# Kernel tuning notes

Hardware: AMD Instinct MI355X
Metric: run time of the kernel (lower is better)

The kernel has to match this reference:

```python
import jax, jax.numpy as jnp
import numpy as np

N = 8192          # total nodes (bipartite: first half left, second half right)
E = 65536         # raw edges
D = 256           # emb_dim
H = 8             # heads
HD = D // H       # head_dim = 32
EAD = 2           # edge_attr_dim


def _init(k, shape, fan_in):
    return (jax.random.normal(k, shape, jnp.float32) / np.sqrt(fan_in)).astype(jnp.float32)


def setup_inputs() -> dict:
    key = jax.random.key(0)
    ks = jax.random.split(key, 16)
    x = jax.random.normal(ks[0], (N, D), jnp.float32)
    src = jax.random.randint(ks[1], (E,), 0, N // 2, jnp.int32)
    dst = jax.random.randint(ks[2], (E,), N // 2, N, jnp.int32)
    edge_index = jnp.stack([src, dst])                       # [2, E]
    edge_attr = jax.random.uniform(ks[3], (E, EAD), jnp.float32)
    query_mask = jax.random.randint(ks[4], (E,), 0, 2, jnp.int32).astype(bool)
    return {
        "x": x,
        "edge_index": edge_index,
        "edge_attr": edge_attr,
        "query_mask": query_mask,
        "start_right": N // 2,
        "W_kqv": _init(ks[5], (D, 3 * D), D), "b_kqv": jnp.zeros((3 * D,), jnp.float32),
        "W_edge": _init(ks[6], (EAD, D), EAD), "b_edge": jnp.zeros((D,), jnp.float32),
        "W_att1": _init(ks[7], (3 * HD, HD), 3 * HD), "b_att1": jnp.zeros((HD,), jnp.float32),
        "W_att2": _init(ks[8], (HD, 1), HD), "b_att2": jnp.zeros((1,), jnp.float32),
        "W_out": _init(ks[9], (D, D), D), "b_out": jnp.zeros((D,), jnp.float32),
        "bn_gamma": jnp.ones((D,), jnp.float32), "bn_beta": jnp.zeros((D,), jnp.float32),
    }


def _build_graph(edge_index, query_mask, n):
    """Replicates MetaGNN.forward edge preprocessing (static, int-only)."""
    ei = np.asarray(edge_index)
    qm = np.asarray(query_mask).astype(bool)
    sup = np.where(~qm)[0]                                   # support edges
    # cat([edge_index[:, support], edge_index.flip(0)], dim=1)
    src = np.concatenate([ei[0, sup], ei[1]])
    dst = np.concatenate([ei[1, sup], ei[0]])
    attr_idx = np.concatenate([sup, np.arange(ei.shape[1])])
    # remove_self_loops
    keep = src != dst
    src, dst, attr_idx = src[keep], dst[keep], attr_idx[keep]
    # add_self_loops with fill_value [0, 0]
    loops = np.arange(n)
    src = np.concatenate([src, loops])
    dst = np.concatenate([dst, loops])
    return jnp.asarray(src), jnp.asarray(dst), jnp.asarray(attr_idx)


def _layer(x, src, dst, ea, W_kqv, b_kqv, W_edge, b_edge, W_att1, b_att1,
           W_att2, b_att2, W_out, b_out, bn_gamma, bn_beta):
    n = x.shape[0]
    kqv = x @ W_kqv + b_kqv                                  # [N, 3D]
    q = kqv[dst, :D].reshape(-1, H, HD)                      # x_i (target)
    k = kqv[src, D:2 * D].reshape(-1, H, HD) / np.sqrt(HD)   # x_j (source)
    v = kqv[src, 2 * D:].reshape(-1, H, HD)
    ef = jax.nn.relu((ea @ W_edge + b_edge).reshape(-1, H, HD))
    feat = jnp.concatenate([k, q, ef], axis=-1)              # [E, H, 3*HD]
    hdn = jax.nn.relu(jnp.einsum('ehf,fd->ehd', feat, W_att1) + b_att1)
    logits = (jnp.einsum('ehd,do->eho', hdn, W_att2) + b_att2)[..., 0]  # [E, H]
    # scatter-softmax over destination node segments
    m = jax.ops.segment_max(logits, dst, num_segments=n)
    a = jnp.exp(logits - m[dst])
    s = jax.ops.segment_sum(a, dst, num_segments=n)
    alpha = a / (s[dst] + 1e-16)                             # [E, H]
    msg = (alpha[..., None] * v).reshape(-1, D) @ W_out + b_out
    out = jax.ops.segment_sum(msg, dst, num_segments=n) + x  # aggr='add' + residual
    # BatchNorm1d (training-mode batch statistics, eps=1e-5)
    mu = out.mean(axis=0)
    var = out.var(axis=0)
    return (out - mu) / jnp.sqrt(var + 1e-5) * bn_gamma + bn_beta


def reference(x, edge_index, edge_attr, query_mask, start_right,
              W_kqv, b_kqv, W_edge, b_edge, W_att1, b_att1, W_att2, b_att2,
              W_out, b_out, bn_gamma, bn_beta):
    n = x.shape[0]
    src, dst, attr_idx = _build_graph(edge_index, query_mask, n)
    ea = jnp.concatenate(
        [edge_attr[attr_idx], jnp.zeros((n, edge_attr.shape[1]), edge_attr.dtype)], axis=0)
    return _layer(x, src, dst, ea, W_kqv, b_kqv, W_edge, b_edge,
                  W_att1, b_att1, W_att2, b_att2, W_out, b_out, bn_gamma, bn_beta)
```

## Files before the change

kernel.cpp:

```cpp
#include <hip/hip_runtime.h>

#define N_NODES 8192
#define E_RAW   65536
#define NSLOT   (2*E_RAW + N_NODES)
#define DEGCAP  48
#define L_ITER  4
#define MAIN_BLKS (E_RAW / (8 * L_ITER))
#define TAIL_BLKS (N_NODES / (8 * L_ITER))

typedef __attribute__((ext_vector_type(8)))  short bf16x8;
typedef __attribute__((ext_vector_type(4)))  short bf16x4;
typedef __attribute__((ext_vector_type(4)))  float f32x4;
typedef __attribute__((ext_vector_type(16))) float f32x16;
typedef unsigned short u16;

__device__ __forceinline__ u16 f2b(float f) {
  unsigned u = __float_as_uint(f);
  u = (u + 0x7FFFu + ((u >> 16) & 1u)) >> 16;
  return (u16)u;
}
__device__ __forceinline__ float b2f(u16 b) {
  return __uint_as_float(((unsigned)b) << 16);
}

__device__ __forceinline__ bf16x4 kq_rd(const char* wbase, int p, int h, int off) {
  int byte = (p*512 + h*64 + off*2) ^ ((p & 7) << 4);
  return *(const bf16x4*)(wbase + byte);
}

__global__ __launch_bounds__(256) void setup_k(
    const float* __restrict__ x, u16* __restrict__ xb,
    const float* __restrict__ W_kqv, const float* __restrict__ b_kqv,
    const float* __restrict__ W_att1, const float* __restrict__ b_att1,
    const float* __restrict__ W_edge, const float* __restrict__ b_edge,
    const float* __restrict__ W_out,
    u16* __restrict__ BcatT, float* __restrict__ biascat,
    u16* __restrict__ wa1t, u16* __restrict__ WoutT, float* __restrict__ beW,
    int4* __restrict__ zbase)
{
  __shared__ float tile[64][65];
  const float inv_sqrt_hd = 0.17677669529663687f;
  int bx = blockIdx.x, t = threadIdx.x;

  if (bx < 2048) {
    int i = bx * 256 + t;
    float4 v = ((const float4*)x)[i];
    ushort4 o;
    o.x = f2b(v.x); o.y = f2b(v.y); o.z = f2b(v.z); o.w = f2b(v.w);
    ((ushort4*)xb)[i] = o;
    return;
  }
  if (bx < 2836) {
    int c = bx - 2048;
    int i = t;
    if (c < 768) {
      float v;
      if (c < 256) {
        int h = c >> 5, d2 = c & 31;
        float s = 0.f;
        #pragma unroll
        for (int j = 0; j < 32; ++j)
          s += W_kqv[i*768 + 256 + h*32 + j] * W_att1[j*32 + d2];
        v = s * inv_sqrt_hd;
      } else if (c < 512) {
        int c2 = c - 256; int h = c2 >> 5, d2 = c2 & 31;
        float s = 0.f;
        #pragma unroll
        for (int j = 0; j < 32; ++j)
          s += W_kqv[i*768 + h*32 + j] * W_att1[(32+j)*32 + d2];
        v = s;
      } else {
        v = W_kqv[i*768 + c];
      }
      BcatT[(size_t)c * 256 + i] = f2b(v);
      if (i == 0) {
        float bv;
        if (c < 256) {
          int h = c >> 5, d2 = c & 31;
          float s = 0.f;
          for (int j = 0; j < 32; ++j)
            s += b_kqv[256 + h*32 + j] * W_att1[j*32 + d2];
          bv = s * inv_sqrt_hd;
        } else if (c < 512) {
          int c2 = c - 256; int h = c2 >> 5, d2 = c2 & 31;
          float s = 0.f;
          for (int j = 0; j < 32; ++j)
            s += b_kqv[h*32 + j] * W_att1[(32+j)*32 + d2];
          bv = s + b_att1[c2 & 31];
        } else {
          bv = b_kqv[c];
        }
        biascat[c] = bv;
      }
    } else if (c < 772) {
      int idx = (c - 768) * 256 + i;
      int d2 = idx >> 5, j = idx & 31;
      wa1t[idx] = f2b(W_att1[(64 + j) * 32 + d2]);
    } else {
      int b = c - 772;
      int r0 = (b >> 2) * 64, c0 = (b & 3) * 64;
      for (int idx = i; idx < 4096; idx += 256) {
        int r = idx >> 6, cc = idx & 63;
        tile[r][cc] = W_out[(size_t)(r0 + r) * 256 + c0 + cc];
      }
      __syncthreads();
      for (int idx = i; idx < 4096; idx += 256) {
        int cc = idx >> 6, r = idx & 63;
        WoutT[(size_t)(c0 + cc) * 256 + r0 + r] = f2b(tile[r][cc]);
      }
    }
    return;
  }
  if (bx == 2836) {
    int h = t >> 5, d2 = t & 31;
    float s = 0.f;
    #pragma unroll
    for (int f = 0; f < 32; ++f)
      s += fmaxf(b_edge[h*32 + f], 0.f) * W_att1[(64 + f)*32 + d2];
    beW[h*32 + d2] = s;
    return;
  }
  int i = (bx - 2837) * 256 + t;
  if (i < 2176) zbase[i] = make_int4(0, 0, 0, 0);
}

__global__ __launch_bounds__(256) void gemm_scatter_k(
    const u16* __restrict__ xb, const u16* __restrict__ BcatT,
    const float* __restrict__ biascat, u16* __restrict__ nodeF,
    const int* __restrict__ ei, const int* __restrict__ qm,
    int* __restrict__ cnt, int* __restrict__ csr)
{
  int bx = blockIdx.x, t = threadIdx.x;
  if (bx < 768) {
    int lane = t & 63, wid = t >> 6;
    int cb = bx % 12, rb = bx / 12;
    int r0 = rb * 128 + wid * 32;
    int c0 = cb * 64;
    int lr = lane & 15, lk = (lane >> 4) * 8;
    f32x4 acc0[4] = {}, acc1[4] = {};
    for (int k0 = 0; k0 < 256; k0 += 32) {
      bf16x8 a0 = *(const bf16x8*)&xb[(size_t)(r0 + lr) * 256 + k0 + lk];
      bf16x8 a1 = *(const bf16x8*)&xb[(size_t)(r0 + 16 + lr) * 256 + k0 + lk];
      bf16x8 b0 = *(const bf16x8*)&BcatT[(size_t)(c0 + lr) * 256 + k0 + lk];
      bf16x8 b1 = *(const bf16x8*)&BcatT[(size_t)(c0 + 16 + lr) * 256 + k0 + lk];
      bf16x8 b2 = *(const bf16x8*)&BcatT[(size_t)(c0 + 32 + lr) * 256 + k0 + lk];
      bf16x8 b3 = *(const bf16x8*)&BcatT[(size_t)(c0 + 48 + lr) * 256 + k0 + lk];
      acc0[0] = __builtin_amdgcn_mfma_f32_16x16x32_bf16(a0, b0, acc0[0], 0, 0, 0);
      acc0[1] = __builtin_amdgcn_mfma_f32_16x16x32_bf16(a0, b1, acc0[1], 0, 0, 0);
      acc0[2] = __builtin_amdgcn_mfma_f32_16x16x32_bf16(a0, b2, acc0[2], 0, 0, 0);
      acc0[3] = __builtin_amdgcn_mfma_f32_16x16x32_bf16(a0, b3, acc0[3], 0, 0, 0);
      acc1[0] = __builtin_amdgcn_mfma_f32_16x16x32_bf16(a1, b0, acc1[0], 0, 0, 0);
      acc1[1] = __builtin_amdgcn_mfma_f32_16x16x32_bf16(a1, b1, acc1[1], 0, 0, 0);
      acc1[2] = __builtin_amdgcn_mfma_f32_16x16x32_bf16(a1, b2, acc1[2], 0, 0, 0);
      acc1[3] = __builtin_amdgcn_mfma_f32_16x16x32_bf16(a1, b3, acc1[3], 0, 0, 0);
    }
    int rbase = r0 + (lane >> 4) * 4;
    #pragma unroll
    for (int cc = 0; cc < 4; ++cc) {
      float bias = biascat[c0 + cc*16 + lr];
      #pragma unroll
      for (int r = 0; r < 4; ++r) {
        nodeF[(size_t)(rbase + r) * 768 + c0 + cc*16 + lr]      = f2b(acc0[cc][r] + bias);
        nodeF[(size_t)(rbase + 16 + r) * 768 + c0 + cc*16 + lr] = f2b(acc1[cc][r] + bias);
      }
    }
    return;
  }
  int slot = (bx - 768) * 256 + t;
  if (slot >= NSLOT) return;
  int src, dst;
  if (slot < E_RAW) {
    if (qm[slot] != 0) return;
    src = ei[slot]; dst = ei[E_RAW + slot];
  } else if (slot < 2*E_RAW) {
    int e = slot - E_RAW;
    src = ei[E_RAW + e]; dst = ei[e];
  } else {
    int n = slot - 2*E_RAW;
    src = n; dst = n;
  }
  int pos = atomicAdd(&cnt[dst], 1);
  if (pos < DEGCAP) csr[dst*DEGCAP + pos] = (slot << 13) | src;
}

__global__ __launch_bounds__(128) void logits_k(
    const int* __restrict__ ei,
    const float* __restrict__ eattr, const u16* __restrict__ nf,
    const u16* __restrict__ wa1t,
    const float* __restrict__ W_edge, const float* __restrict__ b_edge,
    const float* __restrict__ W_att2, const float* __restrict__ beW,
    float* __restrict__ lgd)
{
  __shared__ __align__(16) char kq_raw[2][2][8192];

  int bx = blockIdx.x, t = threadIdx.x, lane = t & 63, wid = t >> 6;
  int col = lane & 31;
  int e = col >> 3, h = col & 7, hi = lane >> 5;

  float w2r[16];
  #pragma unroll
  for (int r = 0; r < 16; ++r)
    w2r[r] = W_att2[(r & 3) + 8*(r >> 2) + 4*hi];

  if (bx < MAIN_BLKS) {
    float ce0[16], ce1[16], cbe[16];
    #pragma unroll
    for (int i = 0; i < 8; ++i) {
      int fA = hi*8 + i, fB = 16 + hi*8 + i;
      ce0[i]   = W_edge[h*32 + fA];       ce0[8+i] = W_edge[h*32 + fB];
      ce1[i]   = W_edge[256 + h*32 + fA]; ce1[8+i] = W_edge[256 + h*32 + fB];
      cbe[i]   = b_edge[h*32 + fA];       cbe[8+i] = b_edge[h*32 + fB];
    }
    bf16x8 af0 = *(const bf16x8*)&wa1t[(lane & 31)*32 + hi*8];
    bf16x8 af1 = *(const bf16x8*)&wa1t[(lane & 31)*32 + 16 + hi*8];

    float2 ea_r[L_ITER];
    int4 nsv[L_ITER], ndv[L_ITER];
    #pragma unroll
    for (int it = 0; it < L_ITER; ++it) {
      int er0 = ((bx * L_ITER + it) * 2 + wid) * 4;
      ea_r[it] = *(const float2*)&eattr[2*(er0 + e)];
      nsv[it] = *(const int4*)&ei[er0];
      ndv[it] = *(const int4*)&ei[E_RAW + er0];
    }

    unsigned lbase = (unsigned)((lane & 31) * 16);
    __builtin_amdgcn_sched_barrier(0);
    {
      char* base = kq_raw[wid][0];
      #pragma unroll
      for (int m = 0; m < 8; ++m) {
        int node = (m >> 2) ? ((&ndv[0].x)[m & 3]) : ((&nsv[0].x)[m & 3]);
        int p = 2*m + hi;
        unsigned goff = lbase ^ (unsigned)((p & 7) << 4);
        const char* src = (const char*)nf + (size_t)node*1536 + (size_t)hi*512 + goff;
        __builtin_amdgcn_global_load_lds(
            (const __attribute__((address_space(1))) void*)src,
            (__attribute__((address_space(3))) void*)(base + m*1024), 16, 0, 0);
      }
    }
    __builtin_amdgcn_sched_barrier(0);

    #pragma unroll
    for (int it = 0; it < L_ITER; ++it) {
      if (it + 1 < L_ITER) {
        char* base = kq_raw[wid][(it + 1) & 1];
        #pragma unroll
        for (int m = 0; m < 8; ++m) {
          int node = (m >> 2) ? ((&ndv[it+1].x)[m & 3]) : ((&nsv[it+1].x)[m & 3]);
          int p = 2*m + hi;
          unsigned goff = lbase ^ (unsigned)((p & 7) << 4);
          const char* src = (const char*)nf + (size_t)node*1536 + (size_t)hi*512 + goff;
          __builtin_amdgcn_global_load_lds(
              (const __attribute__((address_space(1))) void*)src,
              (__attribute__((address_space(3))) void*)(base + m*1024), 16, 0, 0);
        }
      }
      __builtin_amdgcn_sched_barrier(0);

      float2 ea = ea_r[it];
      bf16x8 bf0, bf1;
      #pragma unroll
      for (int i = 0; i < 8; ++i) {
        float v0 = fmaf(ea.x, ce0[i],   fmaf(ea.y, ce1[i],   cbe[i]));
        float v1 = fmaf(ea.x, ce0[8+i], fmaf(ea.y, ce1[8+i], cbe[8+i]));
        bf0[i] = (short)f2b(fmaxf(v0, 0.f));
        bf1[i] = (short)f2b(fmaxf(v1, 0.f));
      }
      f32x16 acc = {};
      acc = __builtin_amdgcn_mfma_f32_32x32x16_bf16(af0, bf0, acc, 0, 0, 0);
      acc = __builtin_amdgcn_mfma_f32_32x32x16_bf16(af1, bf1, acc, 0, 0, 0);

      __builtin_amdgcn_sched_barrier(0);
      if (it + 1 < L_ITER) asm volatile("s_waitcnt vmcnt(8)" ::: "memory");
      else                 asm volatile("s_waitcnt vmcnt(1)" ::: "memory");
      __builtin_amdgcn_sched_barrier(0);

      const char* wbase = kq_raw[wid][it & 1];
      float lg0 = 0.f, lg1 = 0.f;
      #pragma unroll
      for (int q = 0; q < 4; ++q) {
        int off = q*8 + 4*hi;
        bf16x4 k0 = kq_rd(wbase, 2*e,     h, off);
        bf16x4 q0 = kq_rd(wbase, 2*e + 9, h, off);
        bf16x4 k1 = kq_rd(wbase, 2*e + 8, h, off);
        bf16x4 q1 = kq_rd(wbase, 2*e + 1, h, off);
        #pragma unroll
        for (int j = 0; j < 4; ++j) {
          int r = q*4 + j;
          float efw = acc[r];
          float p0 = efw + b2f((u16)k0[j]) + b2f((u16)q0[j]);
          float p1 = efw + b2f((u16)k1[j]) + b2f((u16)q1[j]);
          lg0 = fmaf(fmaxf(p0, 0.f), w2r[r], lg0);
          lg1 = fmaf(fmaxf(p1, 0.f), w2r[r], lg1);
        }
      }
      lg0 += __shfl_xor(lg0, 32);
      lg1 += __shfl_xor(lg1, 32);
      int er = ((bx * L_ITER + it) * 2 + wid) * 4 + e;
      size_t soff = hi ? ((size_t)(E_RAW + er)*8 + h) : ((size_t)er*8 + h);
      lgd[soff] = hi ? lg1 : lg0;
      __builtin_amdgcn_sched_barrier(0);
    }
  } else {
    float bew[16];
    #pragma unroll
    for (int r = 0; r < 16; ++r)
      bew[r] = beW[h*32 + (r & 3) + 8*(r >> 2) + 4*hi];

    unsigned lbase = (unsigned)((lane & 31) * 16);
    char* base = kq_raw[wid][0];
    for (int it = 0; it < L_ITER; ++it) {
      int n0 = (((bx - MAIN_BLKS) * L_ITER + it) * 2 + wid) * 4;
      int nn = n0 + e;
      #pragma unroll
      for (int m = 0; m < 4; ++m) {
        int p = 2*m + hi;
        unsigned goff = lbase ^ (unsigned)((p & 7) << 4);
        const char* src = (const char*)nf + (size_t)(n0 + m)*1536 + (size_t)hi*512 + goff;
        __builtin_amdgcn_global_load_lds(
            (const __attribute__((address_space(1))) void*)src,
            (__attribute__((address_space(3))) void*)(base + m*1024), 16, 0, 0);
      }
      asm volatile("s_waitcnt vmcnt(0)" ::: "memory");
      __builtin_amdgcn_sched_barrier(0);
      float lg0 = 0.f;
      #pragma unroll
      for (int q = 0; q < 4; ++q) {
        int off = q*8 + 4*hi;
        bf16x4 k0 = kq_rd(base, 2*e,     h, off);
        bf16x4 q0 = kq_rd(base, 2*e + 1, h, off);
        #pragma unroll
        for (int j = 0; j < 4; ++j) {
          int r = q*4 + j;
          float p = bew[r] + b2f((u16)k0[j]) + b2f((u16)q0[j]);
          lg0 = fmaf(fmaxf(p, 0.f), w2r[r], lg0);
        }
      }
      lg0 += __shfl_xor(lg0, 32);
      if (hi == 0) lgd[(size_t)(2*E_RAW + nn)*8 + h] = lg0;
      __builtin_amdgcn_sched_barrier(0);
    }
  }
}

__global__ __launch_bounds__(256) void aggr_k(const int* __restrict__ cnt,
                                              const int* __restrict__ csr,
                                              const float* __restrict__ lgd,
                                              const u16* __restrict__ nf,
                                              u16* __restrict__ aggb) {
  int t = threadIdx.x, lane = t & 63, wid = t >> 6;
  int n = blockIdx.x * 4 + wid;
  int deg = cnt[n]; if (deg > DEGCAP) deg = DEGCAP;
  int head = lane >> 3;

  int pk = (lane < deg) ? csr[n*DEGCAP + lane] : 0;

  const u16* vb = nf + 512 + lane * 4;
  int pk0 = __shfl(pk, 0);
  float lg_pf = lgd[(size_t)((unsigned)pk0 >> 13)*8 + head];
  bf16x4 v_pf = *(const bf16x4*)&vb[(size_t)(pk0 & 8191) * 768];

  float m = -3.4e38f, s = 0.f;
  float ac0 = 0.f, ac1 = 0.f, ac2 = 0.f, ac3 = 0.f;
  for (int i = 0; i < deg; ++i) {
    float lgv = lg_pf;
    bf16x4 v = v_pf;
    if (i + 1 < deg) {
      int pkn = __shfl(pk, i + 1);
      lg_pf = lgd[(size_t)((unsigned)pkn >> 13)*8 + head];
      v_pf = *(const bf16x4*)&vb[(size_t)(pkn & 8191) * 768];
    }
    float mn = fmaxf(m, lgv);
    float r = __expf(m - mn);
    float a = __expf(lgv - mn);
    s  = fmaf(s, r, a);
    ac0 = fmaf(ac0, r, a * b2f((u16)v[0]));
    ac1 = fmaf(ac1, r, a * b2f((u16)v[1]));
    ac2 = fmaf(ac2, r, a * b2f((u16)v[2]));
    ac3 = fmaf(ac3, r, a * b2f((u16)v[3]));
    m = mn;
  }
  float sinv = 1.f / (s + 1e-16f);
  ushort4 o;
  o.x = f2b(ac0 * sinv); o.y = f2b(ac1 * sinv);
  o.z = f2b(ac2 * sinv); o.w = f2b(ac3 * sinv);
  *(ushort4*)&aggb[(size_t)n * 256 + lane * 4] = o;
}

__global__ __launch_bounds__(256) void gemmout_k(const u16* __restrict__ aggb,
                                                 const u16* __restrict__ WoutT,
                                                 const float* __restrict__ x,
                                                 const int* __restrict__ cnt,
                                                 const float* __restrict__ b_out,
                                                 float* __restrict__ out,
                                                 float* __restrict__ bnsum,
                                                 float* __restrict__ bnsq) {
  int t = threadIdx.x, lane = t & 63, wid = t >> 6;
  int bx = blockIdx.x;
  int cb = bx & 3, rb = bx >> 2;
  int r0 = rb * 128 + wid * 32;
  int c0 = cb * 64;
  int lr = lane & 15, lk = (lane >> 4) * 8;
  f32x4 acc0[4] = {}, acc1[4] = {};
  for (int k0 = 0; k0 < 256; k0 += 32) {
    bf16x8 a0 = *(const bf16x8*)&aggb[(size_t)(r0 + lr) * 256 + k0 + lk];
    bf16x8 a1 = *(const bf16x8*)&aggb[(size_t)(r0 + 16 + lr) * 256 + k0 + lk];
    bf16x8 b0 = *(const bf16x8*)&WoutT[(size_t)(c0 + lr) * 256 + k0 + lk];
    bf16x8 b1 = *(const bf16x8*)&WoutT[(size_t)(c0 + 16 + lr) * 256 + k0 + lk];
    bf16x8 b2 = *(const bf16x8*)&WoutT[(size_t)(c0 + 32 + lr) * 256 + k0 + lk];
    bf16x8 b3 = *(const bf16x8*)&WoutT[(size_t)(c0 + 48 + lr) * 256 + k0 + lk];
    acc0[0] = __builtin_amdgcn_mfma_f32_16x16x32_bf16(a0, b0, acc0[0], 0, 0, 0);
    acc0[1] = __builtin_amdgcn_mfma_f32_16x16x32_bf16(a0, b1, acc0[1], 0, 0, 0);
    acc0[2] = __builtin_amdgcn_mfma_f32_16x16x32_bf16(a0, b2, acc0[2], 0, 0, 0);
    acc0[3] = __builtin_amdgcn_mfma_f32_16x16x32_bf16(a0, b3, acc0[3], 0, 0, 0);
    acc1[0] = __builtin_amdgcn_mfma_f32_16x16x32_bf16(a1, b0, acc1[0], 0, 0, 0);
    acc1[1] = __builtin_amdgcn_mfma_f32_16x16x32_bf16(a1, b1, acc1[1], 0, 0, 0);
    acc1[2] = __builtin_amdgcn_mfma_f32_16x16x32_bf16(a1, b2, acc1[2], 0, 0, 0);
    acc1[3] = __builtin_amdgcn_mfma_f32_16x16x32_bf16(a1, b3, acc1[3], 0, 0, 0);
  }
  int rbase = r0 + (lane >> 4) * 4;
  float degA[4], degB[4];
  #pragma unroll
  for (int r = 0; r < 4; ++r) {
    degA[r] = (float)cnt[rbase + r];
    degB[r] = (float)cnt[rbase + 16 + r];
  }
  #pragma unroll
  for (int cc = 0; cc < 4; ++cc) {
    int colC = c0 + cc*16 + lr;
    float bC = b_out[colC];
    float sC = 0.f, qC = 0.f;
    #pragma unroll
    for (int r = 0; r < 4; ++r) {
      int rowA = rbase + r, rowB = rbase + 16 + r;
      float v0 = acc0[cc][r] + x[(size_t)rowA * 256 + colC] + degA[r] * bC;
      float v1 = acc1[cc][r] + x[(size_t)rowB * 256 + colC] + degB[r] * bC;
      out[(size_t)rowA * 256 + colC] = v0;
      out[(size_t)rowB * 256 + colC] = v1;
      sC += v0 + v1; qC += v0*v0 + v1*v1;
    }
    #pragma unroll
    for (int msk = 16; msk <= 32; msk <<= 1) {
      sC += __shfl_xor(sC, msk); qC += __shfl_xor(qC, msk);
    }
    if (lane < 16) {
      atomicAdd(&bnsum[colC], sC); atomicAdd(&bnsq[colC], qC);
    }
  }
}

__global__ __launch_bounds__(256) void bnapply_k(float* __restrict__ out,
                                                 const float* __restrict__ bnsum,
                                                 const float* __restrict__ bnsq,
                                                 const float* __restrict__ gamma,
                                                 const float* __restrict__ beta) {
  int t = threadIdx.x;
  int c4 = t & 63;
  int r = blockIdx.x * 4 + (t >> 6);
  float4 s4 = ((const float4*)bnsum)[c4];
  float4 q4 = ((const float4*)bnsq)[c4];
  float4 g4 = ((const float4*)gamma)[c4];
  float4 b4 = ((const float4*)beta)[c4];
  float4 v = ((const float4*)out)[(size_t)r * 64 + c4];
  #pragma unroll
  for (int j = 0; j < 4; ++j) {
    float mu = (&s4.x)[j] * (1.f / 8192.f);
    float var = (&q4.x)[j] * (1.f / 8192.f) - mu*mu;
    float inv = rsqrtf(var + 1e-5f);
    (&v.x)[j] = ((&v.x)[j] - mu) * inv * (&g4.x)[j] + (&b4.x)[j];
  }
  ((float4*)out)[(size_t)r * 64 + c4] = v;
}

extern "C" void kernel_launch(void* const* d_in, const int* in_sizes, int n_in,
                              void* d_out, int out_size, void* d_ws, size_t ws_size,
                              hipStream_t stream) {
  (void)in_sizes; (void)n_in; (void)out_size; (void)ws_size;
  const float* x      = (const float*)d_in[0];
  const int*   ei     = (const int*)d_in[1];
  const float* eattr  = (const float*)d_in[2];
  const int*   qm     = (const int*)d_in[3];
  const float* W_kqv  = (const float*)d_in[5];
  const float* b_kqv  = (const float*)d_in[6];
  const float* W_edge = (const float*)d_in[7];
  const float* b_edge = (const float*)d_in[8];
  const float* W_att1 = (const float*)d_in[9];
  const float* b_att1 = (const float*)d_in[10];
  const float* W_att2 = (const float*)d_in[11];
  const float* W_out  = (const float*)d_in[13];
  const float* b_out  = (const float*)d_in[14];
  const float* gamma  = (const float*)d_in[15];
  const float* beta   = (const float*)d_in[16];
  float* out = (float*)d_out;

  char* w = (char*)d_ws;
  u16*    xb      = (u16*)w;     w += (size_t)N_NODES*256*2;
  u16*    BcatT   = (u16*)w;     w += (size_t)768*256*2;
  u16*    wa1t    = (u16*)w;     w += 1024*2;
  u16*    WoutT   = (u16*)w;     w += (size_t)256*256*2;
  u16*    nodeFb  = (u16*)w;     w += (size_t)N_NODES*768*2;
  float*  biascat = (float*)w;   w += 768*4;
  float*  beW     = (float*)w;   w += 256*4;
  u16*    aggb    = (u16*)w;     w += (size_t)N_NODES*256*2;
  int*    cnt     = (int*)w;     w += N_NODES*4;
  float*  bnsum   = (float*)w;   w += 256*4;
  float*  bnsq    = (float*)w;   w += 256*4;
  int*    csr     = (int*)w;     w += (size_t)N_NODES*DEGCAP*4;
  float*  lgd     = (float*)w;   w += (size_t)NSLOT*8*4;

  setup_k<<<2846, 256, 0, stream>>>(
      x, xb, W_kqv, b_kqv, W_att1, b_att1, W_edge, b_edge, W_out,
      BcatT, biascat, wa1t, WoutT, beW, (int4*)cnt);

  gemm_scatter_k<<<768 + (NSLOT + 255)/256, 256, 0, stream>>>(
      xb, BcatT, biascat, nodeFb, ei, qm, cnt, csr);

  logits_k<<<MAIN_BLKS + TAIL_BLKS, 128, 0, stream>>>(
      ei, eattr, nodeFb, wa1t, W_edge, b_edge, W_att2, beW, lgd);

  aggr_k<<<N_NODES/4, 256, 0, stream>>>(cnt, csr, lgd, nodeFb, aggb);

  gemmout_k<<<256, 256, 0, stream>>>(
      aggb, WoutT, x, cnt, b_out, out, bnsum, bnsq);

  bnapply_k<<<N_NODES/4, 256, 0, stream>>>(out, bnsum, bnsq, gamma, beta);
}
```

Before: 94.94 us.

## Skip unused K/Q half-row loads for query edges in logits kernel

Each wave in logits_k now handles 2 edges per iteration instead of 4, with twice as many iterations. It also reads the query mask, so for query (masked) edges it does not fetch the half of the source/destination feature row whose forward logit is never used. Instead it redirects that load to the half that is needed, which reduces gather traffic. In exchange, half the MFMA columns and lanes compute results that are thrown away, and the LDS buffers and wait counts are retuned to match.

```diff
diff --git a/kernel.cpp b/kernel.cpp
--- a/kernel.cpp
+++ b/kernel.cpp
@@ -4,9 +4,9 @@
 #define E_RAW   65536
 #define NSLOT   (2*E_RAW + N_NODES)
 #define DEGCAP  48
-#define L_ITER  4
-#define MAIN_BLKS (E_RAW / (8 * L_ITER))
-#define TAIL_BLKS (N_NODES / (8 * L_ITER))
+#define L_ITER  8
+#define MAIN_BLKS (E_RAW / (4 * L_ITER))
+#define TAIL_BLKS (N_NODES / (4 * L_ITER))
 
 typedef __attribute__((ext_vector_type(8)))  short bf16x8;
 typedef __attribute__((ext_vector_type(4)))  short bf16x4;
@@ -184,18 +184,19 @@
 }
 
 __global__ __launch_bounds__(128) void logits_k(
-    const int* __restrict__ ei,
+    const int* __restrict__ ei, const int* __restrict__ qm,
     const float* __restrict__ eattr, const u16* __restrict__ nf,
     const u16* __restrict__ wa1t,
     const float* __restrict__ W_edge, const float* __restrict__ b_edge,
     const float* __restrict__ W_att2, const float* __restrict__ beW,
     float* __restrict__ lgd)
 {
-  __shared__ __align__(16) char kq_raw[2][2][8192];
+  __shared__ __align__(16) char kq_raw[2][2][4096];
 
   int bx = blockIdx.x, t = threadIdx.x, lane = t & 63, wid = t >> 6;
   int col = lane & 31;
   int e = col >> 3, h = col & 7, hi = lane >> 5;
+  int je = e & 1;
 
   float w2r[16];
   #pragma unroll
@@ -215,13 +216,14 @@
     bf16x8 af1 = *(const bf16x8*)&wa1t[(lane & 31)*32 + 16 + hi*8];
 
     float2 ea_r[L_ITER];
-    int4 nsv[L_ITER], ndv[L_ITER];
+    int2 nsv[L_ITER], ndv[L_ITER], qmv[L_ITER];
     #pragma unroll
     for (int it = 0; it < L_ITER; ++it) {
-      int er0 = ((bx * L_ITER + it) * 2 + wid) * 4;
-      ea_r[it] = *(const float2*)&eattr[2*(er0 + e)];
-      nsv[it] = *(const int4*)&ei[er0];
-      ndv[it] = *(const int4*)&ei[E_RAW + er0];
+      int er0 = ((bx * L_ITER + it) * 2 + wid) * 2;
+      ea_r[it] = *(const float2*)&eattr[2*(er0 + je)];
+      nsv[it] = *(const int2*)&ei[er0];
+      ndv[it] = *(const int2*)&ei[E_RAW + er0];
+      qmv[it] = *(const int2*)&qm[er0];
     }
 
     unsigned lbase = (unsigned)((lane & 31) * 16);
@@ -229,11 +231,15 @@
     {
       char* base = kq_raw[wid][0];
       #pragma unroll
-      for (int m = 0; m < 8; ++m) {
-        int node = (m >> 2) ? ((&ndv[0].x)[m & 3]) : ((&nsv[0].x)[m & 3]);
+      for (int m = 0; m < 4; ++m) {
+        int ed = m & 1, ty = m >> 1;
+        int node = ty ? ((&ndv[0].x)[ed]) : ((&nsv[0].x)[ed]);
+        int msk = ((&qmv[0].x)[ed]) != 0;
+        int halfsel = ty ? (msk ? 0 : hi) : (msk ? 1 : hi);
         int p = 2*m + hi;
         unsigned goff = lbase ^ (unsigned)((p & 7) << 4);
-        const char* src = (const char*)nf + (size_t)node*1536 + (size_t)hi*512 + goff;
+        const char* src = (const char*)nf + (size_t)node*1536
+                        + (size_t)halfsel*512 + goff;
         __builtin_amdgcn_global_load_lds(
             (const __attribute__((address_space(1))) void*)src,
             (__attribute__((address_space(3))) void*)(base + m*1024), 16, 0, 0);
@@ -246,11 +252,15 @@
       if (it + 1 < L_ITER) {
         char* base = kq_raw[wid][(it + 1) & 1];
         #pragma unroll
-        for (int m = 0; m < 8; ++m) {
-          int node = (m >> 2) ? ((&ndv[it+1].x)[m & 3]) : ((&nsv[it+1].x)[m & 3]);
+        for (int m = 0; m < 4; ++m) {
+          int ed = m & 1, ty = m >> 1;
+          int node = ty ? ((&ndv[it+1].x)[ed]) : ((&nsv[it+1].x)[ed]);
+          int msk = ((&qmv[it+1].x)[ed]) != 0;
+          int halfsel = ty ? (msk ? 0 : hi) : (msk ? 1 : hi);
           int p = 2*m + hi;
           unsigned goff = lbase ^ (unsigned)((p & 7) << 4);
-          const char* src = (const char*)nf + (size_t)node*1536 + (size_t)hi*512 + goff;
+          const char* src = (const char*)nf + (size_t)node*1536
+                          + (size_t)halfsel*512 + goff;
           __builtin_amdgcn_global_load_lds(
               (const __attribute__((address_space(1))) void*)src,
               (__attribute__((address_space(3))) void*)(base + m*1024), 16, 0, 0);
@@ -272,8 +282,9 @@
       acc = __builtin_amdgcn_mfma_f32_32x32x16_bf16(af1, bf1, acc, 0, 0, 0);
 
       __builtin_amdgcn_sched_barrier(0);
-      if (it + 1 < L_ITER) asm volatile("s_waitcnt vmcnt(8)" ::: "memory");
-      else                 asm volatile("s_waitcnt vmcnt(1)" ::: "memory");
+      if (it == 0)              asm volatile("s_waitcnt vmcnt(4)" ::: "memory");
+      else if (it + 1 < L_ITER) asm volatile("s_waitcnt vmcnt(5)" ::: "memory");
+      else                      asm volatile("s_waitcnt vmcnt(1)" ::: "memory");
       __builtin_amdgcn_sched_barrier(0);
 
       const char* wbase = kq_raw[wid][it & 1];
@@ -281,10 +292,10 @@
       #pragma unroll
       for (int q = 0; q < 4; ++q) {
         int off = q*8 + 4*hi;
-        bf16x4 k0 = kq_rd(wbase, 2*e,     h, off);
-        bf16x4 q0 = kq_rd(wbase, 2*e + 9, h, off);
-        bf16x4 k1 = kq_rd(wbase, 2*e + 8, h, off);
-        bf16x4 q1 = kq_rd(wbase, 2*e + 1, h, off);
+        bf16x4 k0 = kq_rd(wbase, 2*je,     h, off);
+        bf16x4 q0 = kq_rd(wbase, 5 + 2*je, h, off);
+        bf16x4 k1 = kq_rd(wbase, 4 + 2*je, h, off);
+        bf16x4 q1 = kq_rd(wbase, 2*je + 1, h, off);
         #pragma unroll
         for (int j = 0; j < 4; ++j) {
           int r = q*4 + j;
@@ -297,9 +308,10 @@
       }
       lg0 += __shfl_xor(lg0, 32);
       lg1 += __shfl_xor(lg1, 32);
-      int er = ((bx * L_ITER + it) * 2 + wid) * 4 + e;
+      int er = ((bx * L_ITER + it) * 2 + wid) * 2 + je;
       size_t soff = hi ? ((size_t)(E_RAW + er)*8 + h) : ((size_t)er*8 + h);
-      lgd[soff] = hi ? lg1 : lg0;
+      float sval = hi ? lg1 : lg0;
+      if (e < 2) lgd[soff] = sval;
       __builtin_amdgcn_sched_barrier(0);
     }
   } else {
@@ -311,13 +323,13 @@
     unsigned lbase = (unsigned)((lane & 31) * 16);
     char* base = kq_raw[wid][0];
     for (int it = 0; it < L_ITER; ++it) {
-      int n0 = (((bx - MAIN_BLKS) * L_ITER + it) * 2 + wid) * 4;
-      int nn = n0 + e;
+      int n0 = (((bx - MAIN_BLKS) * L_ITER + it) * 2 + wid) * 2;
       #pragma unroll
-      for (int m = 0; m < 4; ++m) {
+      for (int m = 0; m < 2; ++m) {
         int p = 2*m + hi;
         unsigned goff = lbase ^ (unsigned)((p & 7) << 4);
-        const char* src = (const char*)nf + (size_t)(n0 + m)*1536 + (size_t)hi*512 + goff;
+        const char* src = (const char*)nf + (size_t)(n0 + m)*1536
+                        + (size_t)hi*512 + goff;
         __builtin_amdgcn_global_load_lds(
             (const __attribute__((address_space(1))) void*)src,
             (__attribute__((address_space(3))) void*)(base + m*1024), 16, 0, 0);
@@ -328,8 +340,8 @@
       #pragma unroll
       for (int q = 0; q < 4; ++q) {
         int off = q*8 + 4*hi;
-        bf16x4 k0 = kq_rd(base, 2*e,     h, off);
-        bf16x4 q0 = kq_rd(base, 2*e + 1, h, off);
+        bf16x4 k0 = kq_rd(base, 2*je,     h, off);
+        bf16x4 q0 = kq_rd(base, 2*je + 1, h, off);
         #pragma unroll
         for (int j = 0; j < 4; ++j) {
           int r = q*4 + j;
@@ -338,7 +350,7 @@
         }
       }
       lg0 += __shfl_xor(lg0, 32);
-      if (hi == 0) lgd[(size_t)(2*E_RAW + nn)*8 + h] = lg0;
+      if (hi == 0 && e < 2) lgd[(size_t)(2*E_RAW + n0 + je)*8 + h] = lg0;
       __builtin_amdgcn_sched_barrier(0);
     }
   }
@@ -517,7 +529,7 @@
       xb, BcatT, biascat, nodeFb, ei, qm, cnt, csr);
 
   logits_k<<<MAIN_BLKS + TAIL_BLKS, 128, 0, stream>>>(
-      ei, eattr, nodeFb, wa1t, W_edge, b_edge, W_att2, beW, lgd);
+      ei, qm, eattr, nodeFb, wa1t, W_edge, b_edge, W_att2, beW, lgd);
 
   aggr_k<<<N_NODES/4, 256, 0, stream>>>(cnt, csr, lgd, nodeFb, aggb);
 
```

Result: slower. 101.9 us (+7.3%).
